# Optimization experiments

Hardware: AMD Instinct MI355X
Metric: run time of the kernel (lower is better)

The kernel has to match this reference:

```python
import jax, jax.numpy as jnp
import numpy as np

D_MODEL = 1024
NUM_HEADS = 16
HEAD_DIM = D_MODEL // NUM_HEADS  # 64
MAX_SEQ_LEN = 2048
BASE = 10000.0


def _rope_tables(seq_len):
    # theta_i = base^(-2i/hd) for i in [0, hd/2)
    theta = 1.0 / (BASE ** (jnp.arange(0, HEAD_DIM, 2, dtype=jnp.float32) / HEAD_DIM))
    angles = jnp.arange(seq_len, dtype=jnp.float32)[:, None] * theta  # [S, hd/2]
    return jnp.cos(angles), jnp.sin(angles)


def _apply_rope(x, cos, sin):
    # x: [B, H, S, hd]; cos/sin: [S, hd/2] broadcast over B,H
    x1 = x[..., 0::2]
    x2 = x[..., 1::2]
    r1 = x1 * cos - x2 * sin
    r2 = x1 * sin + x2 * cos
    return jnp.stack([r1, r2], axis=-1).reshape(x.shape)  # interleave back


def setup_inputs() -> dict:
    key = jax.random.key(0)
    k_x, k_q, k_k, k_v, k_o = jax.random.split(key, 5)
    B, S = 2, 2048
    x = jax.random.normal(k_x, (B, S, D_MODEL), dtype=jnp.float32)
    init = 0.02
    w_q = jax.random.normal(k_q, (D_MODEL, D_MODEL), dtype=jnp.float32) * init
    w_k = jax.random.normal(k_k, (D_MODEL, D_MODEL), dtype=jnp.float32) * init
    w_v = jax.random.normal(k_v, (D_MODEL, D_MODEL), dtype=jnp.float32) * init
    w_o = jax.random.normal(k_o, (D_MODEL, D_MODEL), dtype=jnp.float32) * init
    return {"x": x, "w_q": w_q, "w_k": w_k, "w_v": w_v, "w_o": w_o}


def reference(x, w_q, w_k, w_v, w_o):
    # Prefill path: start_pos=0, cache=None, eval-mode dropout (identity).
    B, S, D = x.shape
    H, hd = NUM_HEADS, HEAD_DIM
    scale = 1.0 / (hd ** 0.5)

    # nn.Linear(bias=False): y = x @ W.T
    q = (x @ w_q.T).reshape(B, S, H, hd).transpose(0, 2, 1, 3)  # [B,H,S,hd]
    k = (x @ w_k.T).reshape(B, S, H, hd).transpose(0, 2, 1, 3)
    v = (x @ w_v.T).reshape(B, S, H, hd).transpose(0, 2, 1, 3)

    cos, sin = _rope_tables(S)  # same tables for every head (per-head torch loop vectorized)
    q_rot = _apply_rope(q, cos, sin)
    k_rot = _apply_rope(k, cos, sin)

    attn = jnp.einsum("bhqd,bhkd->bhqk", q_rot, k_rot) * scale  # [B,H,S,S]
    # causal mask: triu(ones(S,S), diagonal = S_k - S_q + 1 = 1)
    causal = jnp.triu(jnp.ones((S, S), dtype=bool), k=1)
    attn = jnp.where(causal[None, None], -jnp.inf, attn)
    attn_w = jax.nn.softmax(attn, axis=-1)

    out = jnp.einsum("bhqk,bhkd->bhqd", attn_w, v)  # [B,H,S,hd]
    out = out.transpose(0, 2, 1, 3).reshape(B, S, D)
    return out @ w_o.T
```

## Files before the change

kernel.cpp:

```cpp
#include <hip/hip_runtime.h>
#include <hip/hip_bf16.h>
#include <math.h>


#define S_LEN 2048
#define NHEADS 16
#define HD 64
#define DM 1024

typedef __attribute__((ext_vector_type(8))) short bf16x8;
typedef __attribute__((ext_vector_type(4))) float f32x4;

#define MFMA16(a, b, c) __builtin_amdgcn_mfma_f32_16x16x32_bf16((a), (b), (c), 0, 0, 0)
#define NEG_BIG (-1e30f)

__global__ __launch_bounds__(256) void convert_kernel(
    const float* __restrict__ x,  const float* __restrict__ wq,
    const float* __restrict__ wk, const float* __restrict__ wv,
    const float* __restrict__ wo,
    __hip_bfloat16* __restrict__ xb,  __hip_bfloat16* __restrict__ wqb,
    __hip_bfloat16* __restrict__ wkb, __hip_bfloat16* __restrict__ wvb,
    __hip_bfloat16* __restrict__ wob)
{
    const int y = blockIdx.y;
    const float* src;
    __hip_bfloat16* dst;
    size_t off = 0;
    if (y < 4)      { src = x;  dst = xb;  off = (size_t)y * 1048576; }
    else if (y == 4) { src = wq; dst = wqb; }
    else if (y == 5) { src = wk; dst = wkb; }
    else if (y == 6) { src = wv; dst = wvb; }
    else             { src = wo; dst = wob; }

    const size_t i = off + ((size_t)blockIdx.x * 256 + threadIdx.x) * 4;
    float4 v = *(const float4*)(src + i);
    __hip_bfloat16 t[4] = { __float2bfloat16(v.x), __float2bfloat16(v.y),
                            __float2bfloat16(v.z), __float2bfloat16(v.w) };
    *(ushort4*)(dst + i) = *(ushort4*)t;
}

__global__ __launch_bounds__(256) void qkv_kernel(
    const __hip_bfloat16* __restrict__ X,
    const __hip_bfloat16* __restrict__ Wq,
    const __hip_bfloat16* __restrict__ Wk,
    const __hip_bfloat16* __restrict__ Wv,
    __hip_bfloat16* __restrict__ qws,
    __hip_bfloat16* __restrict__ kws,
    __hip_bfloat16* __restrict__ vws)
{
    const int z = blockIdx.z;
    const __hip_bfloat16* __restrict__ W = (z == 0) ? Wq : (z == 1) ? Wk : Wv;
    __hip_bfloat16* __restrict__ out = (z == 0) ? qws : (z == 1) ? kws : vws;

    constexpr int LDK = 40;
    __shared__ __align__(16) __hip_bfloat16 Asm[128 * LDK];
    __shared__ __align__(16) __hip_bfloat16 Bsm[128 * LDK];

    const int tid = threadIdx.x;
    const int wave = tid >> 6, lane = tid & 63;
    const int quad = lane >> 4, l15 = lane & 15;
    const int wm = (wave >> 1) * 64, wn = (wave & 1) * 64;
    const int m0 = blockIdx.y * 128, n0 = blockIdx.x * 128;

    f32x4 acc[4][4] = {};

    for (int k0 = 0; k0 < DM; k0 += 32) {
#pragma unroll
        for (int c = 0; c < 2; c++) {
            int idx = c * 2048 + tid * 8;
            int r = idx >> 5, kc = idx & 31;
            *(int4*)(&Asm[r * LDK + kc]) = *(const int4*)(X + (size_t)(m0 + r) * DM + k0 + kc);
            *(int4*)(&Bsm[r * LDK + kc]) = *(const int4*)(W + (size_t)(n0 + r) * DM + k0 + kc);
        }
        __syncthreads();
        bf16x8 af[4], bfv[4];
#pragma unroll
        for (int i = 0; i < 4; i++)
            af[i] = *(const bf16x8*)(&Asm[(wm + i * 16 + l15) * LDK + quad * 8]);
#pragma unroll
        for (int j = 0; j < 4; j++)
            bfv[j] = *(const bf16x8*)(&Bsm[(wn + j * 16 + l15) * LDK + quad * 8]);
#pragma unroll
        for (int i = 0; i < 4; i++)
#pragma unroll
            for (int j = 0; j < 4; j++)
                acc[i][j] = MFMA16(af[i], bfv[j], acc[i][j]);
        __syncthreads();
    }

#pragma unroll
    for (int i = 0; i < 4; i++) {
#pragma unroll
        for (int r = 0; r < 4; r++) {
            int m = m0 + wm + i * 16 + quad * 4 + r;
            int b = m >> 11, s = m & 2047;
#pragma unroll
            for (int j = 0; j < 4; j++) {
                int col = n0 + wn + j * 16 + l15;
                int h = col >> 6, d = col & 63;
                size_t idx = (z == 2)
                    ? (((size_t)(b * NHEADS + h)) * HD + d) * S_LEN + s
                    : (((size_t)(b * NHEADS + h)) * S_LEN + s) * HD + d;
                out[idx] = __float2bfloat16(acc[i][j][r]);
            }
        }
    }
}

__global__ __launch_bounds__(256) void rope_kernel(
    __hip_bfloat16* __restrict__ q, __hip_bfloat16* __restrict__ k)
{
    __hip_bfloat16* __restrict__ p = (blockIdx.y == 0) ? q : k;
    const float qscale = (blockIdx.y == 0) ? 0.125f : 1.0f;
    const int gid = blockIdx.x * 256 + threadIdx.x;
    const int e0 = gid * 8;
    const int s = (gid >> 3) & 2047;
    const int d0 = (gid & 7) * 8;

    int4 raw = *(const int4*)(p + e0);
    __hip_bfloat16* v = (__hip_bfloat16*)&raw;
#pragma unroll
    for (int i = 0; i < 4; i++) {
        int pi = (d0 >> 1) + i;
        float theta = powf(10000.0f, -(float)(2 * pi) * (1.0f / 64.0f));
        float sn, cs;
        sincosf((float)s * theta, &sn, &cs);
        float x1 = __bfloat162float(v[2 * i]);
        float x2 = __bfloat162float(v[2 * i + 1]);
        v[2 * i]     = __float2bfloat16((x1 * cs - x2 * sn) * qscale);
        v[2 * i + 1] = __float2bfloat16((x1 * sn + x2 * cs) * qscale);
    }
    *(int4*)(p + e0) = raw;
}


#define SMPV(sc, mm, ll, oo, Pr)                                               \
    do {                                                                       \
        float pm[4];                                                           \
        _Pragma("unroll")                                                      \
        for (int r = 0; r < 4; r++)                                            \
            pm[r] = fmaxf(fmaxf(sc[0][r], sc[1][r]),                           \
                          fmaxf(sc[2][r], sc[3][r]));                          \
        bool ok = true;                                                        \
        _Pragma("unroll")                                                      \
        for (int r = 0; r < 4; r++) ok = ok && (pm[r] <= mm[r] + 8.0f);        \
        if (!__all(ok)) {                                                      \
            _Pragma("unroll")                                                  \
            for (int off = 1; off < 16; off <<= 1)                             \
                _Pragma("unroll")                                              \
                for (int r = 0; r < 4; r++)                                    \
                    pm[r] = fmaxf(pm[r], __shfl_xor(pm[r], off));              \
            _Pragma("unroll")                                                  \
            for (int r = 0; r < 4; r++) {                                      \
                float mn = fmaxf(mm[r], pm[r]);                                \
                float al = __expf(mm[r] - mn);                                 \
                mm[r] = mn;                                                    \
                ll[r] *= al;                                                   \
                _Pragma("unroll")                                              \
                for (int t = 0; t < 4; t++) oo[t][r] *= al;                    \
            }                                                                  \
        }                                                                      \
        _Pragma("unroll")                                                      \
        for (int t = 0; t < 4; t++)                                            \
            _Pragma("unroll")                                                  \
            for (int r = 0; r < 4; r++)                                        \
                Pr[(quad * 4 + r) * 72 + t * 16 + l15] =                       \
                    __float2bfloat16(__expf(sc[t][r] - mm[r]));                \
        _Pragma("unroll")                                                      \
        for (int st = 0; st < 2; st++) {                                       \
            bf16x8 pf = *(const bf16x8*)(&Pr[l15 * 72 + st * 32 + quad * 8]);  \
            __builtin_amdgcn_s_setprio(1);                                     \
            ll = MFMA16(pf, ones, ll);                                         \
            _Pragma("unroll")                                                  \
            for (int t = 0; t < 4; t++) oo[t] = MFMA16(pf, vf[st][t], oo[t]);  \
            __builtin_amdgcn_s_setprio(0);                                     \
        }                                                                      \
    } while (0)

#define LOAD_VF(kv0)                                                           \
    do {                                                                       \
        _Pragma("unroll")                                                      \
        for (int st = 0; st < 2; st++)                                         \
            _Pragma("unroll")                                                  \
            for (int t = 0; t < 4; t++)                                        \
                vf[st][t] = *(const bf16x8*)(Vtb +                             \
                    (size_t)(t * 16 + l15) * S_LEN + (kv0) + st * 32 + quad * 8); \
    } while (0)

#define LOAD_KF(kv0)                                                           \
    do {                                                                       \
        _Pragma("unroll")                                                      \
        for (int st = 0; st < 2; st++)                                         \
            _Pragma("unroll")                                                  \
            for (int t = 0; t < 4; t++)                                        \
                kf[st][t] = *(const bf16x8*)(Kb +                              \
                    (size_t)((kv0) + t * 16 + l15) * HD + st * 32 + quad * 8); \
    } while (0)

#define QK(sc, qf)                                                             \
    do {                                                                       \
        __builtin_amdgcn_s_setprio(1);                                         \
        _Pragma("unroll")                                                      \
        for (int st = 0; st < 2; st++)                                         \
            _Pragma("unroll")                                                  \
            for (int t = 0; t < 4; t++) sc[t] = MFMA16(qf[st], kf[st][t], sc[t]); \
        __builtin_amdgcn_s_setprio(0);                                         \
    } while (0)

#define MASK(sc, rowbase, kv0)                                                 \
    do {                                                                       \
        _Pragma("unroll")                                                      \
        for (int t = 0; t < 4; t++) {                                          \
            int col = (kv0) + t * 16 + l15;                                    \
            _Pragma("unroll")                                                  \
            for (int r = 0; r < 4; r++) {                                      \
                int row = (rowbase) + quad * 4 + r;                            \
                if (col > row) sc[t][r] = NEG_BIG;                             \
            }                                                                  \
        }                                                                      \
    } while (0)

__global__ __launch_bounds__(256) void attn_kernel(
    const __hip_bfloat16* __restrict__ Qg,
    const __hip_bfloat16* __restrict__ Kg,
    const __hip_bfloat16* __restrict__ Vtg,
    __hip_bfloat16* __restrict__ Og)
{
    const int bh = blockIdx.x;
    const int qi = (blockIdx.y < 8) ? blockIdx.y : 23 - blockIdx.y;
    const int tid = threadIdx.x;
    const int w = tid >> 6, lane = tid & 63;
    const int quad = lane >> 4, l15 = lane & 15;
    const size_t base = (size_t)bh * S_LEN * HD;
    const __hip_bfloat16* Qb = Qg + base;
    const __hip_bfloat16* Kb = Kg + base;
    const __hip_bfloat16* Vtb = Vtg + base;
    const int b = bh >> 4, h = bh & 15;

    __shared__ __align__(16) __hip_bfloat16 Pl[128 * 72];
    __hip_bfloat16* PrA = &Pl[w * 32 * 72];
    __hip_bfloat16* PrB = PrA + 16 * 72;

    const int q0 = qi * 128;
    const int rowA = q0 + w * 16;
    const int rowB = rowA + 64;

    bf16x8 qfA[2], qfB[2];
#pragma unroll
    for (int st = 0; st < 2; st++) {
        qfA[st] = *(const bf16x8*)(Qb + (size_t)(rowA + l15) * HD + st * 32 + quad * 8);
        qfB[st] = *(const bf16x8*)(Qb + (size_t)(rowB + l15) * HD + st * 32 + quad * 8);
    }

    bf16x8 ones;
#pragma unroll
    for (int i = 0; i < 8; i++) ones[i] = (short)0x3F80;

    float mA[4], mB[4];
    f32x4 lA = {}, lB = {};
    f32x4 oA[4] = {}, oB[4] = {};
#pragma unroll
    for (int r = 0; r < 4; r++) { mA[r] = NEG_BIG; mB[r] = NEG_BIG; }

    bf16x8 kf[2][4];
    bf16x8 vf[2][4];
    LOAD_KF(0);

#pragma unroll 1
    for (int j = 0; j < 2 * qi; j++) {
        const int kv0 = j * 64;
        LOAD_VF(kv0);
        f32x4 scA[4] = {}, scB[4] = {};
        QK(scA, qfA);
        QK(scB, qfB);
        LOAD_KF(kv0 + 64);
        SMPV(scA, mA, lA, oA, PrA);
        SMPV(scB, mB, lB, oB, PrB);
    }

    {
        const int kv0 = q0;
        LOAD_VF(kv0);
        f32x4 scA[4] = {}, scB[4] = {};
        QK(scA, qfA);
        QK(scB, qfB);
        LOAD_KF(kv0 + 64);
        MASK(scA, rowA, kv0);
        SMPV(scA, mA, lA, oA, PrA);
        SMPV(scB, mB, lB, oB, PrB);
    }

    {
        const int kv0 = q0 + 64;
        LOAD_VF(kv0);
        f32x4 scB[4] = {};
        QK(scB, qfB);
        MASK(scB, rowB, kv0);
        SMPV(scB, mB, lB, oB, PrB);
    }

#pragma unroll
    for (int t = 0; t < 4; t++)
#pragma unroll
        for (int r = 0; r < 4; r++) {
            int d = t * 16 + l15;
            int sA = rowA + quad * 4 + r;
            Og[((size_t)(b * S_LEN + sA)) * DM + h * HD + d] =
                __float2bfloat16(oA[t][r] / lA[r]);
            int sB = rowB + quad * 4 + r;
            Og[((size_t)(b * S_LEN + sB)) * DM + h * HD + d] =
                __float2bfloat16(oB[t][r] / lB[r]);
        }
}

__global__ __launch_bounds__(256) void oproj_kernel(
    const __hip_bfloat16* __restrict__ A,
    const __hip_bfloat16* __restrict__ W,
    float* __restrict__ out)
{
    constexpr int LDK = 40;
    __shared__ __align__(16) __hip_bfloat16 Asm[128 * LDK];
    __shared__ __align__(16) __hip_bfloat16 Bsm[128 * LDK];

    const int tid = threadIdx.x;
    const int wave = tid >> 6, lane = tid & 63;
    const int quad = lane >> 4, l15 = lane & 15;
    const int wm = (wave >> 1) * 64, wn = (wave & 1) * 64;
    const int m0 = blockIdx.y * 128, n0 = blockIdx.x * 128;

    f32x4 acc[4][4] = {};

    for (int k0 = 0; k0 < DM; k0 += 32) {
#pragma unroll
        for (int c = 0; c < 2; c++) {
            int idx = c * 2048 + tid * 8;
            int r = idx >> 5, kc = idx & 31;
            *(int4*)(&Asm[r * LDK + kc]) = *(const int4*)(A + (size_t)(m0 + r) * DM + k0 + kc);
            *(int4*)(&Bsm[r * LDK + kc]) = *(const int4*)(W + (size_t)(n0 + r) * DM + k0 + kc);
        }
        __syncthreads();
        bf16x8 af[4], bfv[4];
#pragma unroll
        for (int i = 0; i < 4; i++)
            af[i] = *(const bf16x8*)(&Asm[(wm + i * 16 + l15) * LDK + quad * 8]);
#pragma unroll
        for (int j = 0; j < 4; j++)
            bfv[j] = *(const bf16x8*)(&Bsm[(wn + j * 16 + l15) * LDK + quad * 8]);
#pragma unroll
        for (int i = 0; i < 4; i++)
#pragma unroll
            for (int j = 0; j < 4; j++)
                acc[i][j] = MFMA16(af[i], bfv[j], acc[i][j]);
        __syncthreads();
    }

#pragma unroll
    for (int i = 0; i < 4; i++)
#pragma unroll
        for (int r = 0; r < 4; r++) {
            int m = m0 + wm + i * 16 + quad * 4 + r;
#pragma unroll
            for (int j = 0; j < 4; j++) {
                int col = n0 + wn + j * 16 + l15;
                __hip_bfloat16 bb = __float2bfloat16(acc[i][j][r]);
                unsigned int u = ((unsigned int)(*(unsigned short*)&bb)) << 16;
                out[(size_t)m * DM + col] = __uint_as_float(u);
            }
        }
}

extern "C" void kernel_launch(void* const* d_in, const int* in_sizes, int n_in,
                              void* d_out, int out_size, void* d_ws, size_t ws_size,
                              hipStream_t stream)
{
    const float* x  = (const float*)d_in[0];
    const float* wq = (const float*)d_in[1];
    const float* wk = (const float*)d_in[2];
    const float* wv = (const float*)d_in[3];
    const float* wo = (const float*)d_in[4];
    float* out = (float*)d_out;

    const size_t xe = (size_t)2 * S_LEN * DM;
    const size_t we = (size_t)DM * DM;
    __hip_bfloat16* xb  = (__hip_bfloat16*)d_ws;
    __hip_bfloat16* wqb = xb + xe;
    __hip_bfloat16* wkb = wqb + we;
    __hip_bfloat16* wvb = wkb + we;
    __hip_bfloat16* wob = wvb + we;
    __hip_bfloat16* qws = wob + we;
    __hip_bfloat16* kws = qws + xe;
    __hip_bfloat16* vws = kws + xe;
    __hip_bfloat16* aws = vws + xe;

    dim3 blk(256, 1, 1);
    convert_kernel<<<dim3(1024, 8, 1), blk, 0, stream>>>(x, wq, wk, wv, wo,
                                                         xb, wqb, wkb, wvb, wob);
    qkv_kernel<<<dim3(8, 32, 3), blk, 0, stream>>>(xb, wqb, wkb, wvb, qws, kws, vws);
    rope_kernel<<<dim3(2048, 2, 1), blk, 0, stream>>>(qws, kws);
    attn_kernel<<<dim3(32, 16, 1), blk, 0, stream>>>(qws, kws, vws, aws);
    oproj_kernel<<<dim3(8, 32, 1), blk, 0, stream>>>(aws, wob, out);
}
```

Measured before the change: 237.7 us.

## Use direct global-to-LDS loads in GEMMs, precompute RoPE table, fold log2e into softmax

```diff
diff --git a/kernel.cpp b/kernel.cpp
--- a/kernel.cpp
+++ b/kernel.cpp
@@ -13,6 +13,11 @@
 
 #define MFMA16(a, b, c) __builtin_amdgcn_mfma_f32_16x16x32_bf16((a), (b), (c), 0, 0, 0)
 #define NEG_BIG (-1e30f)
+
+#define GLOAD_LDS16(g, l)                                                      \
+    __builtin_amdgcn_global_load_lds(                                          \
+        (const __attribute__((address_space(1))) void*)(g),                    \
+        (__attribute__((address_space(3))) void*)(l), 16, 0, 0)
 
 __global__ __launch_bounds__(256) void convert_kernel(
     const float* __restrict__ x,  const float* __restrict__ wq,
@@ -20,9 +25,20 @@
     const float* __restrict__ wo,
     __hip_bfloat16* __restrict__ xb,  __hip_bfloat16* __restrict__ wqb,
     __hip_bfloat16* __restrict__ wkb, __hip_bfloat16* __restrict__ wvb,
-    __hip_bfloat16* __restrict__ wob)
+    __hip_bfloat16* __restrict__ wob, float2* __restrict__ tab)
 {
     const int y = blockIdx.y;
+    if (y == 8) {
+        const int gid = blockIdx.x * 256 + threadIdx.x;
+        if (gid < S_LEN * 32) {
+            const int s = gid >> 5, p = gid & 31;
+            float theta = powf(10000.0f, -(float)(2 * p) * (1.0f / 64.0f));
+            float sn, cs;
+            sincosf((float)s * theta, &sn, &cs);
+            tab[gid] = make_float2(cs, sn);
+        }
+        return;
+    }
     const float* src;
     __hip_bfloat16* dst;
     size_t off = 0;
@@ -52,9 +68,8 @@
     const __hip_bfloat16* __restrict__ W = (z == 0) ? Wq : (z == 1) ? Wk : Wv;
     __hip_bfloat16* __restrict__ out = (z == 0) ? qws : (z == 1) ? kws : vws;
 
-    constexpr int LDK = 40;
-    __shared__ __align__(16) __hip_bfloat16 Asm[128 * LDK];
-    __shared__ __align__(16) __hip_bfloat16 Bsm[128 * LDK];
+    __shared__ __align__(16) __hip_bfloat16 Asm[128 * 32];
+    __shared__ __align__(16) __hip_bfloat16 Bsm[128 * 32];
 
     const int tid = threadIdx.x;
     const int wave = tid >> 6, lane = tid & 63;
@@ -69,17 +84,17 @@
         for (int c = 0; c < 2; c++) {
             int idx = c * 2048 + tid * 8;
             int r = idx >> 5, kc = idx & 31;
-            *(int4*)(&Asm[r * LDK + kc]) = *(const int4*)(X + (size_t)(m0 + r) * DM + k0 + kc);
-            *(int4*)(&Bsm[r * LDK + kc]) = *(const int4*)(W + (size_t)(n0 + r) * DM + k0 + kc);
+            GLOAD_LDS16(X + (size_t)(m0 + r) * DM + k0 + kc, &Asm[idx]);
+            GLOAD_LDS16(W + (size_t)(n0 + r) * DM + k0 + kc, &Bsm[idx]);
         }
         __syncthreads();
         bf16x8 af[4], bfv[4];
 #pragma unroll
         for (int i = 0; i < 4; i++)
-            af[i] = *(const bf16x8*)(&Asm[(wm + i * 16 + l15) * LDK + quad * 8]);
+            af[i] = *(const bf16x8*)(&Asm[(wm + i * 16 + l15) * 32 + quad * 8]);
 #pragma unroll
         for (int j = 0; j < 4; j++)
-            bfv[j] = *(const bf16x8*)(&Bsm[(wn + j * 16 + l15) * LDK + quad * 8]);
+            bfv[j] = *(const bf16x8*)(&Bsm[(wn + j * 16 + l15) * 32 + quad * 8]);
 #pragma unroll
         for (int i = 0; i < 4; i++)
 #pragma unroll
@@ -108,27 +123,31 @@
 }
 
 __global__ __launch_bounds__(256) void rope_kernel(
-    __hip_bfloat16* __restrict__ q, __hip_bfloat16* __restrict__ k)
+    __hip_bfloat16* __restrict__ q, __hip_bfloat16* __restrict__ k,
+    const float2* __restrict__ tab)
 {
     __hip_bfloat16* __restrict__ p = (blockIdx.y == 0) ? q : k;
-    const float qscale = (blockIdx.y == 0) ? 0.125f : 1.0f;
+    const float qscale = (blockIdx.y == 0) ? 0.18033688011112042f
+                                           : 1.0f;
     const int gid = blockIdx.x * 256 + threadIdx.x;
     const int e0 = gid * 8;
     const int s = (gid >> 3) & 2047;
-    const int d0 = (gid & 7) * 8;
+    const int p4 = (gid & 7) * 4;
+
+    const float2* tp = tab + s * 32 + p4;
+    float4 t01 = *(const float4*)(tp);
+    float4 t23 = *(const float4*)(tp + 2);
+    float cs[4] = { t01.x, t01.z, t23.x, t23.z };
+    float sn[4] = { t01.y, t01.w, t23.y, t23.w };
 
     int4 raw = *(const int4*)(p + e0);
     __hip_bfloat16* v = (__hip_bfloat16*)&raw;
 #pragma unroll
     for (int i = 0; i < 4; i++) {
-        int pi = (d0 >> 1) + i;
-        float theta = powf(10000.0f, -(float)(2 * pi) * (1.0f / 64.0f));
-        float sn, cs;
-        sincosf((float)s * theta, &sn, &cs);
         float x1 = __bfloat162float(v[2 * i]);
         float x2 = __bfloat162float(v[2 * i + 1]);
-        v[2 * i]     = __float2bfloat16((x1 * cs - x2 * sn) * qscale);
-        v[2 * i + 1] = __float2bfloat16((x1 * sn + x2 * cs) * qscale);
+        v[2 * i]     = __float2bfloat16((x1 * cs[i] - x2 * sn[i]) * qscale);
+        v[2 * i + 1] = __float2bfloat16((x1 * sn[i] + x2 * cs[i]) * qscale);
     }
     *(int4*)(p + e0) = raw;
 }
@@ -143,7 +162,7 @@
                           fmaxf(sc[2][r], sc[3][r]));                          \
         bool ok = true;                                                        \
         _Pragma("unroll")                                                      \
-        for (int r = 0; r < 4; r++) ok = ok && (pm[r] <= mm[r] + 8.0f);        \
+        for (int r = 0; r < 4; r++) ok = ok && (pm[r] <= mm[r] + 11.0f);       \
         if (!__all(ok)) {                                                      \
             _Pragma("unroll")                                                  \
             for (int off = 1; off < 16; off <<= 1)                             \
@@ -153,7 +172,7 @@
             _Pragma("unroll")                                                  \
             for (int r = 0; r < 4; r++) {                                      \
                 float mn = fmaxf(mm[r], pm[r]);                                \
-                float al = __expf(mm[r] - mn);                                 \
+                float al = exp2f(mm[r] - mn);                                  \
                 mm[r] = mn;                                                    \
                 ll[r] *= al;                                                   \
                 _Pragma("unroll")                                              \
@@ -165,7 +184,7 @@
             _Pragma("unroll")                                                  \
             for (int r = 0; r < 4; r++)                                        \
                 Pr[(quad * 4 + r) * 72 + t * 16 + l15] =                       \
-                    __float2bfloat16(__expf(sc[t][r] - mm[r]));                \
+                    __float2bfloat16(exp2f(sc[t][r] - mm[r]));                 \
         _Pragma("unroll")                                                      \
         for (int st = 0; st < 2; st++) {                                       \
             bf16x8 pf = *(const bf16x8*)(&Pr[l15 * 72 + st * 32 + quad * 8]);  \
@@ -318,9 +337,8 @@
     const __hip_bfloat16* __restrict__ W,
     float* __restrict__ out)
 {
-    constexpr int LDK = 40;
-    __shared__ __align__(16) __hip_bfloat16 Asm[128 * LDK];
-    __shared__ __align__(16) __hip_bfloat16 Bsm[128 * LDK];
+    __shared__ __align__(16) __hip_bfloat16 Asm[128 * 32];
+    __shared__ __align__(16) __hip_bfloat16 Bsm[128 * 32];
 
     const int tid = threadIdx.x;
     const int wave = tid >> 6, lane = tid & 63;
@@ -335,17 +353,17 @@
         for (int c = 0; c < 2; c++) {
             int idx = c * 2048 + tid * 8;
             int r = idx >> 5, kc = idx & 31;
-            *(int4*)(&Asm[r * LDK + kc]) = *(const int4*)(A + (size_t)(m0 + r) * DM + k0 + kc);
-            *(int4*)(&Bsm[r * LDK + kc]) = *(const int4*)(W + (size_t)(n0 + r) * DM + k0 + kc);
+            GLOAD_LDS16(A + (size_t)(m0 + r) * DM + k0 + kc, &Asm[idx]);
+            GLOAD_LDS16(W + (size_t)(n0 + r) * DM + k0 + kc, &Bsm[idx]);
         }
         __syncthreads();
         bf16x8 af[4], bfv[4];
 #pragma unroll
         for (int i = 0; i < 4; i++)
-            af[i] = *(const bf16x8*)(&Asm[(wm + i * 16 + l15) * LDK + quad * 8]);
+            af[i] = *(const bf16x8*)(&Asm[(wm + i * 16 + l15) * 32 + quad * 8]);
 #pragma unroll
         for (int j = 0; j < 4; j++)
-            bfv[j] = *(const bf16x8*)(&Bsm[(wn + j * 16 + l15) * LDK + quad * 8]);
+            bfv[j] = *(const bf16x8*)(&Bsm[(wn + j * 16 + l15) * 32 + quad * 8]);
 #pragma unroll
         for (int i = 0; i < 4; i++)
 #pragma unroll
@@ -391,12 +409,13 @@
     __hip_bfloat16* kws = qws + xe;
     __hip_bfloat16* vws = kws + xe;
     __hip_bfloat16* aws = vws + xe;
+    float2* tab = (float2*)aws;
 
     dim3 blk(256, 1, 1);
-    convert_kernel<<<dim3(1024, 8, 1), blk, 0, stream>>>(x, wq, wk, wv, wo,
-                                                         xb, wqb, wkb, wvb, wob);
+    convert_kernel<<<dim3(1024, 9, 1), blk, 0, stream>>>(x, wq, wk, wv, wo,
+                                                         xb, wqb, wkb, wvb, wob, tab);
     qkv_kernel<<<dim3(8, 32, 3), blk, 0, stream>>>(xb, wqb, wkb, wvb, qws, kws, vws);
-    rope_kernel<<<dim3(2048, 2, 1), blk, 0, stream>>>(qws, kws);
+    rope_kernel<<<dim3(2048, 2, 1), blk, 0, stream>>>(qws, kws, tab);
     attn_kernel<<<dim3(32, 16, 1), blk, 0, stream>>>(qws, kws, vws, aws);
     oproj_kernel<<<dim3(8, 32, 1), blk, 0, stream>>>(aws, wob, out);
 }
```

Measured after the change: 216.2 us. -9.0%, faster.
